# Kernel tuning notes

Measured on AMD Instinct MI355X. Metric: run time of the kernel, lower is better.

## Reference

```python
import jax, jax.numpy as jnp
import numpy as np


def gin_conv(h, src, dst, w1, w2):
    # GINConv, eps=0: mlp(x_i + sum_{j->i} x_j); PyG flow source->target
    agg = jax.ops.segment_sum(h[src], dst, num_segments=h.shape[0])
    z = h + agg
    # create_mlp: Linear(no bias) -> ReLU -> Linear(no bias)
    return jnp.maximum(z @ w1, 0.0) @ w2


def setup_inputs() -> dict:
    N, E, FEAT, D, L, G, OUT = 50000, 800000, 128, 128, 3, 256, 256
    key = jax.random.key(0)
    ks = jax.random.split(key, 8)
    x = jax.random.normal(ks[0], (N, FEAT), jnp.float32)
    edge_index = jax.random.randint(ks[1], (2, E), 0, N, jnp.int32)
    batch_index = jnp.sort(jax.random.randint(ks[2], (N,), 0, G, jnp.int32))
    init = lambda k, shp, fan: jax.random.normal(k, shp, jnp.float32) * np.float32(1.0 / np.sqrt(fan))
    w1_0 = init(ks[3], (FEAT, D), FEAT)
    w2_0 = init(ks[4], (D, D), D)
    gin_w1 = init(ks[5], (L - 1, D, D), D)
    gin_w2 = init(ks[6], (L - 1, D, D), D)
    out_w = init(ks[7], (3 * D, OUT), 3 * D)
    out_b = jnp.zeros((OUT,), jnp.float32)
    return dict(x=x, edge_index=edge_index, batch_index=batch_index,
                w1_0=w1_0, w2_0=w2_0, gin_w1=gin_w1, gin_w2=gin_w2,
                out_w=out_w, out_b=out_b, num_graphs=G)


def reference(x, edge_index, batch_index, w1_0, w2_0, gin_w1, gin_w2, out_w, out_b, num_graphs):
    src, dst = edge_index[0], edge_index[1]
    # dropout is identity in eval mode; batchnorm is unused in the original forward
    h = jnp.maximum(gin_conv(x, src, dst, w1_0, w2_0), 0.0)
    for i in range(gin_w1.shape[0]):  # small fixed layer count
        h = jnp.maximum(gin_conv(h, src, dst, gin_w1[i], gin_w2[i]), 0.0)
    # multi-pool readout: [gmp | gap | gadp]
    gsum = jax.ops.segment_sum(h, batch_index, num_segments=num_graphs)
    cnt = jax.ops.segment_sum(jnp.ones((h.shape[0], 1), h.dtype), batch_index, num_segments=num_graphs)
    gmean = gsum / jnp.maximum(cnt, 1.0)
    gmax = jax.ops.segment_max(h, batch_index, num_segments=num_graphs)
    pooled = jnp.concatenate([gmax, gmean, gsum], axis=1)  # [G, 3*D]
    return pooled @ out_w + out_b
```

## Files before the change

kernel.cpp:

```cpp
#include <hip/hip_runtime.h>

#define DD 128
#define BIN_CH 2048

typedef __attribute__((ext_vector_type(8))) short short8;
typedef __attribute__((ext_vector_type(4))) float f32x4;

__device__ __forceinline__ unsigned short f2bf(float x) {
  unsigned int b = __float_as_uint(x);
  b += 0x7fffu + ((b >> 16) & 1u);
  return (unsigned short)(b >> 16);
}

__device__ __forceinline__ unsigned int cvt_pk_bf16(float lo, float hi) {
  unsigned int d;
  asm("v_cvt_pk_bf16_f32 %0, %1, %2" : "=v"(d) : "v"(lo), "v"(hi));
  return d;
}

__global__ __launch_bounds__(256) void bhist_kernel(const int* __restrict__ dst,
                                                    int* __restrict__ cnt, int E, int NB) {
  __shared__ int lh[256];
  const int t = threadIdx.x;
  lh[t] = 0;
  __syncthreads();
  const int e4 = E >> 2;
  const int4* d4 = (const int4*)dst;
  for (int i = blockIdx.x * 256 + t; i < e4; i += gridDim.x * 256) {
    int4 v = d4[i];
    atomicAdd(&lh[v.x >> 8], 1);
    atomicAdd(&lh[v.y >> 8], 1);
    atomicAdd(&lh[v.z >> 8], 1);
    atomicAdd(&lh[v.w >> 8], 1);
  }
  if (blockIdx.x == 0) {
    for (int i = (e4 << 2) + t; i < E; i += 256) atomicAdd(&lh[dst[i] >> 8], 1);
  }
  __syncthreads();
  if (t < NB && lh[t]) atomicAdd(&cnt[t], lh[t]);
}

__global__ __launch_bounds__(256) void bscan_kernel(const int* __restrict__ cnt,
                                                    int* __restrict__ bucket_base,
                                                    int* __restrict__ cursor,
                                                    int* __restrict__ offs, int NB, int N) {
  __shared__ int s[256];
  const int t = threadIdx.x;
  int v = (t < NB) ? cnt[t] : 0;
  s[t] = v;
  __syncthreads();
#pragma unroll
  for (int o = 1; o < 256; o <<= 1) {
    int u = (t >= o) ? s[t - o] : 0;
    __syncthreads();
    s[t] += u;
    __syncthreads();
  }
  if (t < NB) {
    bucket_base[t] = s[t] - v;
    cursor[t] = s[t] - v;
  }
  if (t == 255) {
    bucket_base[NB] = s[255];
    offs[N] = s[255];
  }
}

__global__ __launch_bounds__(256) void bin_kernel(const int* __restrict__ src,
                                                  const int* __restrict__ dst,
                                                  int* __restrict__ cursor,
                                                  unsigned int* __restrict__ binned,
                                                  int E, int NB) {
  __shared__ int lcount[256], lbase[256], lcur[256], lgbase[256], sscan[256];
  __shared__ unsigned int stage[BIN_CH];
  const int t = threadIdx.x;
  const int cb = blockIdx.x * BIN_CH;
  lcount[t] = 0;
  __syncthreads();

  int sv[BIN_CH / 256], dv[BIN_CH / 256];
#pragma unroll
  for (int i = 0; i < BIN_CH / 256; ++i) {
    const int idx = cb + i * 256 + t;
    if (idx < E) {
      sv[i] = src[idx];
      dv[i] = dst[idx];
      atomicAdd(&lcount[dv[i] >> 8], 1);
    } else {
      sv[i] = -1;
    }
  }
  __syncthreads();
  sscan[t] = lcount[t];
  __syncthreads();
#pragma unroll
  for (int o = 1; o < 256; o <<= 1) {
    int u = (t >= o) ? sscan[t - o] : 0;
    __syncthreads();
    sscan[t] += u;
    __syncthreads();
  }
  lbase[t] = sscan[t] - lcount[t];
  lcur[t] = lbase[t];
  __syncthreads();
#pragma unroll
  for (int i = 0; i < BIN_CH / 256; ++i) {
    if (sv[i] >= 0) {
      const int b = dv[i] >> 8;
      const int pos = atomicAdd(&lcur[b], 1);
      stage[pos] = (unsigned)sv[i] | ((unsigned)(dv[i] & 255) << 16) | ((unsigned)b << 24);
    }
  }
  __syncthreads();
  if (t < NB && lcount[t]) lgbase[t] = atomicAdd(&cursor[t], lcount[t]);
  __syncthreads();
  const int total = (cb + BIN_CH <= E) ? BIN_CH : (E - cb);
  for (int idx = t; idx < total; idx += 256) {
    const unsigned int rec = stage[idx];
    const int b = rec >> 24;
    binned[lgbase[b] + (idx - lbase[b])] = rec;
  }
}

__global__ __launch_bounds__(256) void build_kernel(const unsigned int* __restrict__ binned,
                                                    const int* __restrict__ bucket_base,
                                                    int* __restrict__ csr,
                                                    int* __restrict__ offs, int N) {
  __shared__ int ncount[256], ncur[256], sscan[256];
  const int b = blockIdx.x;
  const int t = threadIdx.x;
  const int nstart = b << 8;
  const int rb = bucket_base[b], re = bucket_base[b + 1];
  ncount[t] = 0;
  __syncthreads();
  for (int idx = rb + t; idx < re; idx += 256)
    atomicAdd(&ncount[(binned[idx] >> 16) & 255], 1);
  __syncthreads();
  sscan[t] = ncount[t];
  __syncthreads();
#pragma unroll
  for (int o = 1; o < 256; o <<= 1) {
    int u = (t >= o) ? sscan[t - o] : 0;
    __syncthreads();
    sscan[t] += u;
    __syncthreads();
  }
  const int excl = sscan[t] - ncount[t];
  ncur[t] = excl;
  if (nstart + t < N) offs[nstart + t] = rb + excl;
  __syncthreads();
  for (int idx = rb + t; idx < re; idx += 256) {
    const unsigned int rec = binned[idx];
    const int p = atomicAdd(&ncur[(rec >> 16) & 255], 1);
    csr[rb + p] = (int)(rec & 0xffffu);
  }
}

__global__ __launch_bounds__(256) void cvt_x_kernel(const float* __restrict__ X,
                                                    unsigned int* __restrict__ Xb, int n4) {
  int i = blockIdx.x * 256 + threadIdx.x;
  if (i >= n4) return;
  float4 v = ((const float4*)X)[i];
  uint2 o;
  o.x = cvt_pk_bf16(v.x, v.y);
  o.y = cvt_pk_bf16(v.z, v.w);
  ((uint2*)Xb)[i] = o;
}

__global__ __launch_bounds__(256) void pack_w_kernel(const float* __restrict__ W,
                                                     unsigned short* __restrict__ P,
                                                     int nmats) {
  int q = blockIdx.x * 256 + threadIdx.x;
  if (q >= nmats * 16384) return;
  int mat = q >> 14;
  int r = q & 16383;
  int e = r & 7, l = (r >> 3) & 63, ks = (r >> 9) & 3, ct = r >> 11;
  int k = ks * 32 + (l >> 4) * 8 + e;
  int n = ct * 16 + (l & 15);
  P[q] = f2bf(W[(size_t)mat * 16384 + k * DD + n]);
}

__global__ __launch_bounds__(256) void pack_wo_kernel(const float* __restrict__ W,
                                                      unsigned short* __restrict__ P) {
  int q = blockIdx.x * 256 + threadIdx.x;
  if (q >= 384 * 256) return;
  int e = q & 7, l = (q >> 3) & 63;
  int rest = q >> 9;
  int ks = rest % 12, ct = rest / 12;
  int k = ks * 32 + (l >> 4) * 8 + e;
  int n = ct * 16 + (l & 15);
  P[q] = f2bf(W[(size_t)k * 256 + n]);
}

__device__ __forceinline__ void bfacc8(float* a, uint4 v) {
  a[0] += __uint_as_float(v.x << 16);
  a[1] += __uint_as_float(v.x & 0xffff0000u);
  a[2] += __uint_as_float(v.y << 16);
  a[3] += __uint_as_float(v.y & 0xffff0000u);
  a[4] += __uint_as_float(v.z << 16);
  a[5] += __uint_as_float(v.z & 0xffff0000u);
  a[6] += __uint_as_float(v.w << 16);
  a[7] += __uint_as_float(v.w & 0xffff0000u);
}

__global__ __launch_bounds__(256) void gin_layer_kernel(
    const uint4* __restrict__ H4, const int* __restrict__ offs,
    const int* __restrict__ csr_src,
    const unsigned short* __restrict__ W1p,
    const unsigned short* __restrict__ W2p,
    unsigned short* __restrict__ Hout, int N) {
  __shared__ unsigned short zl[32 * DD];
  __shared__ unsigned short h1[32 * DD];
  const int t = threadIdx.x;
  const int w = t >> 6;
  const int l = t & 63;
  const int qw = l >> 4;
  const int ql = l & 15;
  const int row0 = blockIdx.x * 32;

#pragma unroll
  for (int i = 0; i < 8; ++i) {
    const int mrow = w * 8 + i;
    const int node = row0 + mrow;
    float acc[8] = {0.f, 0.f, 0.f, 0.f, 0.f, 0.f, 0.f, 0.f};
    if (node < N) {
      if (qw == 0) bfacc8(acc, H4[(size_t)node * 16 + ql]);
      const int e1 = offs[node + 1];
      int e = offs[node] + qw;
      for (; e + 4 < e1; e += 8) {
        uint4 a = H4[(size_t)csr_src[e] * 16 + ql];
        uint4 b = H4[(size_t)csr_src[e + 4] * 16 + ql];
        bfacc8(acc, a);
        bfacc8(acc, b);
      }
      if (e < e1) bfacc8(acc, H4[(size_t)csr_src[e] * 16 + ql]);
    }
#pragma unroll
    for (int j = 0; j < 8; ++j) {
      acc[j] += __shfl_xor(acc[j], 16, 64);
      acc[j] += __shfl_xor(acc[j], 32, 64);
    }
    if (qw == 0) {
      uint4 o;
      o.x = cvt_pk_bf16(acc[0], acc[1]);
      o.y = cvt_pk_bf16(acc[2], acc[3]);
      o.z = cvt_pk_bf16(acc[4], acc[5]);
      o.w = cvt_pk_bf16(acc[6], acc[7]);
      *(uint4*)&zl[mrow * DD + ((ql ^ (mrow & 7)) << 3)] = o;
    }
  }
  __syncthreads();

  const int m_a = l & 15;
  const int g = l >> 4;

  f32x4 acc1[2][2];
#pragma unroll
  for (int t2 = 0; t2 < 2; ++t2)
#pragma unroll
    for (int j = 0; j < 2; ++j) acc1[t2][j] = (f32x4){0.f, 0.f, 0.f, 0.f};

#pragma unroll
  for (int ks = 0; ks < 4; ++ks) {
    const int c8 = ks * 4 + g;
    short8 a0 = *(const short8*)&zl[m_a * DD + ((c8 ^ (m_a & 7)) << 3)];
    short8 a1 = *(const short8*)&zl[(16 + m_a) * DD + ((c8 ^ (m_a & 7)) << 3)];
#pragma unroll
    for (int j = 0; j < 2; ++j) {
      const int ct = w * 2 + j;
      short8 b = *(const short8*)&W1p[(size_t)((ct * 4 + ks) * 64 + l) * 8];
      acc1[0][j] = __builtin_amdgcn_mfma_f32_16x16x32_bf16(a0, b, acc1[0][j], 0, 0, 0);
      acc1[1][j] = __builtin_amdgcn_mfma_f32_16x16x32_bf16(a1, b, acc1[1][j], 0, 0, 0);
    }
  }
#pragma unroll
  for (int t2 = 0; t2 < 2; ++t2)
#pragma unroll
    for (int j = 0; j < 2; ++j) {
      const int c = (w * 2 + j) * 16 + m_a;
#pragma unroll
      for (int r = 0; r < 4; r += 2) {
        unsigned int p = cvt_pk_bf16(fmaxf(acc1[t2][j][r], 0.f),
                                     fmaxf(acc1[t2][j][r + 1], 0.f));
        const int m0 = t2 * 16 + g * 4 + r;
        const int m1 = m0 + 1;
        h1[m0 * DD + (((c >> 3) ^ (m0 & 7)) << 3) + (c & 7)] = (unsigned short)p;
        h1[m1 * DD + (((c >> 3) ^ (m1 & 7)) << 3) + (c & 7)] = (unsigned short)(p >> 16);
      }
    }
  __syncthreads();

  f32x4 acc2[2][2];
#pragma unroll
  for (int t2 = 0; t2 < 2; ++t2)
#pragma unroll
    for (int j = 0; j < 2; ++j) acc2[t2][j] = (f32x4){0.f, 0.f, 0.f, 0.f};

#pragma unroll
  for (int ks = 0; ks < 4; ++ks) {
    const int c8 = ks * 4 + g;
    short8 a0 = *(const short8*)&h1[m_a * DD + ((c8 ^ (m_a & 7)) << 3)];
    short8 a1 = *(const short8*)&h1[(16 + m_a) * DD + ((c8 ^ (m_a & 7)) << 3)];
#pragma unroll
    for (int j = 0; j < 2; ++j) {
      const int ct = w * 2 + j;
      short8 b = *(const short8*)&W2p[(size_t)((ct * 4 + ks) * 64 + l) * 8];
      acc2[0][j] = __builtin_amdgcn_mfma_f32_16x16x32_bf16(a0, b, acc2[0][j], 0, 0, 0);
      acc2[1][j] = __builtin_amdgcn_mfma_f32_16x16x32_bf16(a1, b, acc2[1][j], 0, 0, 0);
    }
  }
#pragma unroll
  for (int t2 = 0; t2 < 2; ++t2)
#pragma unroll
    for (int j = 0; j < 2; ++j) {
      const int c = (w * 2 + j) * 16 + m_a;
#pragma unroll
      for (int r = 0; r < 4; r += 2) {
        unsigned int p = cvt_pk_bf16(fmaxf(acc2[t2][j][r], 0.f),
                                     fmaxf(acc2[t2][j][r + 1], 0.f));
        const int m0 = t2 * 16 + g * 4 + r;
        const int m1 = m0 + 1;
        zl[m0 * DD + (((c >> 3) ^ (m0 & 7)) << 3) + (c & 7)] = (unsigned short)p;
        zl[m1 * DD + (((c >> 3) ^ (m1 & 7)) << 3) + (c & 7)] = (unsigned short)(p >> 16);
      }
    }
  __syncthreads();

#pragma unroll
  for (int it = 0; it < 2; ++it) {
    const int q = t + it * 256;
    const int m = q >> 4;
    const int c8 = q & 15;
    short8 v = *(const short8*)&zl[m * DD + ((c8 ^ (m & 7)) << 3)];
    *(short8*)(Hout + (size_t)(row0 + m) * DD + c8 * 8) = v;
  }
}

__device__ __forceinline__ int lower_bound_dev(const int* a, int n, int v) {
  int lo = 0, hi = n;
  while (lo < hi) {
    int mid = (lo + hi) >> 1;
    if (a[mid] < v) lo = mid + 1; else hi = mid;
  }
  return lo;
}

__global__ __launch_bounds__(256) void pool_kernel(const unsigned int* __restrict__ H2,
                                                   const int* __restrict__ batch,
                                                   unsigned int* __restrict__ pooled_bf,
                                                   int N) {
  const int g = blockIdx.x;
  __shared__ int sRange[2];
  if (threadIdx.x < 2) sRange[threadIdx.x] = lower_bound_dev(batch, N, g + threadIdx.x);
  __syncthreads();
  const int lo = sRange[0], hi = sRange[1];
  const int cp = threadIdx.x & 63;
  const int sl = threadIdx.x >> 6;
  float sx = 0.f, sy = 0.f, mx = 0.f, my = 0.f;
  for (int r = lo + sl; r < hi; r += 4) {
    unsigned int u = H2[(size_t)r * 64 + cp];
    float a = __uint_as_float(u << 16);
    float b = __uint_as_float(u & 0xffff0000u);
    sx += a; sy += b;
    mx = fmaxf(mx, a); my = fmaxf(my, b);
  }
  __shared__ float sS[3][DD], sM[3][DD];
  if (sl > 0) {
    sS[sl - 1][cp * 2] = sx; sS[sl - 1][cp * 2 + 1] = sy;
    sM[sl - 1][cp * 2] = mx; sM[sl - 1][cp * 2 + 1] = my;
  }
  __syncthreads();
  if (sl == 0) {
#pragma unroll
    for (int j = 0; j < 3; ++j) {
      sx += sS[j][cp * 2]; sy += sS[j][cp * 2 + 1];
      mx = fmaxf(mx, sM[j][cp * 2]); my = fmaxf(my, sM[j][cp * 2 + 1]);
    }
    const float cnt = fmaxf((float)(hi - lo), 1.f);
    const size_t pb = (size_t)g * 192;
    pooled_bf[pb + cp] = cvt_pk_bf16(mx, my);
    pooled_bf[pb + 64 + cp] = cvt_pk_bf16(sx / cnt, sy / cnt);
    pooled_bf[pb + 128 + cp] = cvt_pk_bf16(sx, sy);
  }
}

__global__ __launch_bounds__(256) void final_mfma_kernel(const unsigned short* __restrict__ Pb,
                                                         const unsigned short* __restrict__ Wop,
                                                         const float* __restrict__ bo,
                                                         float* __restrict__ out, int G) {
  const int w = threadIdx.x >> 6;
  const int l = threadIdx.x & 63;
  const int rt = blockIdx.x >> 2;
  const int cg = blockIdx.x & 3;
  const int ct = cg * 4 + w;
  const int row0 = rt * 16;
  const int m_a = l & 15;
  const int g = l >> 4;

  f32x4 acc = (f32x4){0.f, 0.f, 0.f, 0.f};
#pragma unroll
  for (int ks = 0; ks < 12; ++ks) {
    short8 a = *(const short8*)&Pb[((size_t)(row0 + m_a) * 384) + ks * 32 + g * 8];
    short8 b = *(const short8*)&Wop[(size_t)((ct * 12 + ks) * 64 + l) * 8];
    acc = __builtin_amdgcn_mfma_f32_16x16x32_bf16(a, b, acc, 0, 0, 0);
  }

  const int n = ct * 16 + m_a;
  const float bias = bo[n];
#pragma unroll
  for (int r = 0; r < 4; ++r) {
    const int row = row0 + g * 4 + r;
    if (row < G) out[(size_t)row * 256 + n] = acc[r] + bias;
  }
}

extern "C" void kernel_launch(void* const* d_in, const int* in_sizes, int n_in,
                              void* d_out, int out_size, void* d_ws, size_t ws_size,
                              hipStream_t stream) {
  const float* x     = (const float*)d_in[0];
  const int*   ei    = (const int*)d_in[1];
  const int*   batch = (const int*)d_in[2];
  const float* w1_0  = (const float*)d_in[3];
  const float* w2_0  = (const float*)d_in[4];
  const float* gw1   = (const float*)d_in[5];
  const float* gw2   = (const float*)d_in[6];
  const float* out_w = (const float*)d_in[7];
  const float* out_b = (const float*)d_in[8];

  const int N   = in_sizes[0] / DD;
  const int E   = in_sizes[1] / 2;
  const int Lm1 = in_sizes[5] / (DD * DD);
  const int OUT = in_sizes[7] / (3 * DD);
  const int G   = out_size / OUT;

  const int* src = ei;
  const int* dst = ei + E;
  const int NB = (N + 255) >> 8;
  const int nmats = 2 + 2 * Lm1;
  const int Npad = (N + 31) & ~31;
  const int Gpad = (G + 15) & ~15;

  char* p = (char*)d_ws;
  auto take = [&](size_t bytes) -> char* {
    char* r = p;
    p += (bytes + 511) & ~(size_t)511;
    return r;
  };
  int* cnt         = (int*)take((size_t)NB * 4);
  int* bucket_base = (int*)take((size_t)(NB + 1) * 4);
  int* cursor      = (int*)take((size_t)NB * 4);
  unsigned int* binned = (unsigned int*)take((size_t)E * 4);
  int* csr         = (int*)take((size_t)E * 4);
  int* offs        = (int*)take((size_t)(N + 1) * 4);
  unsigned short* packW = (unsigned short*)take((size_t)nmats * 16384 * 2);
  unsigned short* packWo = (unsigned short*)take((size_t)384 * 256 * 2);
  unsigned short* xb    = (unsigned short*)take((size_t)Npad * DD * 2);
  unsigned short* bufA  = (unsigned short*)take((size_t)Npad * DD * 2);
  unsigned short* bufB  = (unsigned short*)take((size_t)Npad * DD * 2);
  unsigned int* pooled_bf = (unsigned int*)take((size_t)Gpad * 192 * 4);

  pack_w_kernel<<<(1 * 16384 + 255) / 256, 256, 0, stream>>>(w1_0, packW, 1);
  pack_w_kernel<<<(1 * 16384 + 255) / 256, 256, 0, stream>>>(w2_0, packW + 16384, 1);
  pack_w_kernel<<<(Lm1 * 16384 + 255) / 256, 256, 0, stream>>>(gw1, packW + 2 * 16384, Lm1);
  pack_w_kernel<<<(Lm1 * 16384 + 255) / 256, 256, 0, stream>>>(gw2, packW + (size_t)(2 + Lm1) * 16384, Lm1);
  pack_wo_kernel<<<(384 * 256 + 255) / 256, 256, 0, stream>>>(out_w, packWo);
  cvt_x_kernel<<<(N * DD / 4 + 255) / 256, 256, 0, stream>>>(x, (unsigned int*)xb, N * DD / 4);

  hipMemsetAsync(cnt, 0, (size_t)NB * 4, stream);
  bhist_kernel<<<196, 256, 0, stream>>>(dst, cnt, E, NB);
  bscan_kernel<<<1, 256, 0, stream>>>(cnt, bucket_base, cursor, offs, NB, N);
  bin_kernel<<<(E + BIN_CH - 1) / BIN_CH, 256, 0, stream>>>(src, dst, cursor, binned, E, NB);
  build_kernel<<<NB, 256, 0, stream>>>(binned, bucket_base, csr, offs, N);

  const int ntiles32 = Npad / 32;
  const unsigned short* hcur = xb;
  unsigned short* bufs[2] = {bufA, bufB};
  for (int l = 0; l <= Lm1; ++l) {
    unsigned short* hout = bufs[l & 1];
    const unsigned short* W1p = packW + (size_t)((l == 0) ? 0 : (2 + (l - 1))) * 16384;
    const unsigned short* W2p = packW + (size_t)((l == 0) ? 1 : (2 + Lm1 + (l - 1))) * 16384;
    gin_layer_kernel<<<ntiles32, 256, 0, stream>>>(
        (const uint4*)hcur, offs, csr, W1p, W2p, hout, N);
    hcur = hout;
  }

  pool_kernel<<<G, 256, 0, stream>>>((const unsigned int*)hcur, batch, pooled_bf, N);
  final_mfma_kernel<<<(Gpad / 16) * 4, 256, 0, stream>>>(
      (const unsigned short*)pooled_bf, packWo, out_b, (float*)d_out, G);
}
```

Before: 191.0 us.

## Fuse prep kernels, store CSR as 16-bit, and give each row its own 16-lane group

```diff
diff --git a/kernel.cpp b/kernel.cpp
--- a/kernel.cpp
+++ b/kernel.cpp
@@ -124,7 +124,7 @@
 
 __global__ __launch_bounds__(256) void build_kernel(const unsigned int* __restrict__ binned,
                                                     const int* __restrict__ bucket_base,
-                                                    int* __restrict__ csr,
+                                                    unsigned short* __restrict__ csr16,
                                                     int* __restrict__ offs, int N) {
   __shared__ int ncount[256], ncur[256], sscan[256];
   const int b = blockIdx.x;
@@ -152,44 +152,54 @@
   for (int idx = rb + t; idx < re; idx += 256) {
     const unsigned int rec = binned[idx];
     const int p = atomicAdd(&ncur[(rec >> 16) & 255], 1);
-    csr[rb + p] = (int)(rec & 0xffffu);
-  }
-}
-
-__global__ __launch_bounds__(256) void cvt_x_kernel(const float* __restrict__ X,
-                                                    unsigned int* __restrict__ Xb, int n4) {
-  int i = blockIdx.x * 256 + threadIdx.x;
-  if (i >= n4) return;
-  float4 v = ((const float4*)X)[i];
-  uint2 o;
-  o.x = cvt_pk_bf16(v.x, v.y);
-  o.y = cvt_pk_bf16(v.z, v.w);
-  ((uint2*)Xb)[i] = o;
-}
-
-__global__ __launch_bounds__(256) void pack_w_kernel(const float* __restrict__ W,
-                                                     unsigned short* __restrict__ P,
-                                                     int nmats) {
+    csr16[rb + p] = (unsigned short)(rec & 0xffffu);
+  }
+}
+
+__global__ __launch_bounds__(256) void prep_kernel(
+    const float* __restrict__ x, const float* __restrict__ w1_0,
+    const float* __restrict__ w2_0, const float* __restrict__ gw1,
+    const float* __restrict__ gw2, const float* __restrict__ out_w,
+    unsigned int* __restrict__ xb, unsigned short* __restrict__ packW,
+    unsigned short* __restrict__ packWo, int* __restrict__ cnt,
+    int n4, int nmats, int Lm1, int NB) {
   int q = blockIdx.x * 256 + threadIdx.x;
-  if (q >= nmats * 16384) return;
-  int mat = q >> 14;
-  int r = q & 16383;
-  int e = r & 7, l = (r >> 3) & 63, ks = (r >> 9) & 3, ct = r >> 11;
-  int k = ks * 32 + (l >> 4) * 8 + e;
-  int n = ct * 16 + (l & 15);
-  P[q] = f2bf(W[(size_t)mat * 16384 + k * DD + n]);
-}
-
-__global__ __launch_bounds__(256) void pack_wo_kernel(const float* __restrict__ W,
-                                                      unsigned short* __restrict__ P) {
-  int q = blockIdx.x * 256 + threadIdx.x;
-  if (q >= 384 * 256) return;
-  int e = q & 7, l = (q >> 3) & 63;
-  int rest = q >> 9;
-  int ks = rest % 12, ct = rest / 12;
-  int k = ks * 32 + (l >> 4) * 8 + e;
-  int n = ct * 16 + (l & 15);
-  P[q] = f2bf(W[(size_t)k * 256 + n]);
+  if (q < n4) {
+    float4 v = ((const float4*)x)[q];
+    uint2 o;
+    o.x = cvt_pk_bf16(v.x, v.y);
+    o.y = cvt_pk_bf16(v.z, v.w);
+    ((uint2*)xb)[q] = o;
+    return;
+  }
+  q -= n4;
+  const int npack = nmats * 16384;
+  if (q < npack) {
+    const int mat = q >> 14;
+    const float* W;
+    if (mat == 0) W = w1_0;
+    else if (mat == 1) W = w2_0;
+    else if (mat < 2 + Lm1) W = gw1 + (size_t)(mat - 2) * 16384;
+    else W = gw2 + (size_t)(mat - 2 - Lm1) * 16384;
+    const int r = q & 16383;
+    const int e = r & 7, l = (r >> 3) & 63, ks = (r >> 9) & 3, ct = r >> 11;
+    const int k = ks * 32 + (l >> 4) * 8 + e;
+    const int n = ct * 16 + (l & 15);
+    packW[q] = f2bf(W[(size_t)k * DD + n]);
+    return;
+  }
+  q -= npack;
+  if (q < 384 * 256) {
+    const int e = q & 7, l = (q >> 3) & 63;
+    const int rest = q >> 9;
+    const int ks = rest % 12, ct = rest / 12;
+    const int k = ks * 32 + (l >> 4) * 8 + e;
+    const int n = ct * 16 + (l & 15);
+    packWo[q] = f2bf(out_w[(size_t)k * 256 + n]);
+    return;
+  }
+  q -= 384 * 256;
+  if (q < NB) cnt[q] = 0;
 }
 
 __device__ __forceinline__ void bfacc8(float* a, uint4 v) {
@@ -205,52 +215,49 @@
 
 __global__ __launch_bounds__(256) void gin_layer_kernel(
     const uint4* __restrict__ H4, const int* __restrict__ offs,
-    const int* __restrict__ csr_src,
+    const unsigned short* __restrict__ csr16,
     const unsigned short* __restrict__ W1p,
     const unsigned short* __restrict__ W2p,
     unsigned short* __restrict__ Hout, int N) {
   __shared__ unsigned short zl[32 * DD];
   __shared__ unsigned short h1[32 * DD];
   const int t = threadIdx.x;
-  const int w = t >> 6;
-  const int l = t & 63;
-  const int qw = l >> 4;
-  const int ql = l & 15;
+  const int quarter = t >> 4;
+  const int ql = t & 15;
   const int row0 = blockIdx.x * 32;
 
 #pragma unroll
-  for (int i = 0; i < 8; ++i) {
-    const int mrow = w * 8 + i;
+  for (int i = 0; i < 2; ++i) {
+    const int mrow = quarter + i * 16;
     const int node = row0 + mrow;
     float acc[8] = {0.f, 0.f, 0.f, 0.f, 0.f, 0.f, 0.f, 0.f};
     if (node < N) {
-      if (qw == 0) bfacc8(acc, H4[(size_t)node * 16 + ql]);
+      bfacc8(acc, H4[(size_t)node * 16 + ql]);
       const int e1 = offs[node + 1];
-      int e = offs[node] + qw;
-      for (; e + 4 < e1; e += 8) {
-        uint4 a = H4[(size_t)csr_src[e] * 16 + ql];
-        uint4 b = H4[(size_t)csr_src[e + 4] * 16 + ql];
+      int e = offs[node];
+      for (; e + 3 < e1; e += 4) {
+        uint4 a = H4[(size_t)csr16[e] * 16 + ql];
+        uint4 b = H4[(size_t)csr16[e + 1] * 16 + ql];
+        uint4 c = H4[(size_t)csr16[e + 2] * 16 + ql];
+        uint4 d = H4[(size_t)csr16[e + 3] * 16 + ql];
         bfacc8(acc, a);
         bfacc8(acc, b);
+        bfacc8(acc, c);
+        bfacc8(acc, d);
       }
-      if (e < e1) bfacc8(acc, H4[(size_t)csr_src[e] * 16 + ql]);
-    }
-#pragma unroll
-    for (int j = 0; j < 8; ++j) {
-      acc[j] += __shfl_xor(acc[j], 16, 64);
-      acc[j] += __shfl_xor(acc[j], 32, 64);
-    }
-    if (qw == 0) {
-      uint4 o;
-      o.x = cvt_pk_bf16(acc[0], acc[1]);
-      o.y = cvt_pk_bf16(acc[2], acc[3]);
-      o.z = cvt_pk_bf16(acc[4], acc[5]);
-      o.w = cvt_pk_bf16(acc[6], acc[7]);
-      *(uint4*)&zl[mrow * DD + ((ql ^ (mrow & 7)) << 3)] = o;
-    }
-  }
-  __syncthreads();
-
+      for (; e < e1; ++e) bfacc8(acc, H4[(size_t)csr16[e] * 16 + ql]);
+    }
+    uint4 o;
+    o.x = cvt_pk_bf16(acc[0], acc[1]);
+    o.y = cvt_pk_bf16(acc[2], acc[3]);
+    o.z = cvt_pk_bf16(acc[4], acc[5]);
+    o.w = cvt_pk_bf16(acc[6], acc[7]);
+    *(uint4*)&zl[mrow * DD + ((ql ^ (mrow & 7)) << 3)] = o;
+  }
+  __syncthreads();
+
+  const int w = t >> 6;
+  const int l = t & 63;
   const int m_a = l & 15;
   const int g = l >> 4;
 
@@ -450,7 +457,7 @@
   int* bucket_base = (int*)take((size_t)(NB + 1) * 4);
   int* cursor      = (int*)take((size_t)NB * 4);
   unsigned int* binned = (unsigned int*)take((size_t)E * 4);
-  int* csr         = (int*)take((size_t)E * 4);
+  unsigned short* csr16 = (unsigned short*)take((size_t)E * 2);
   int* offs        = (int*)take((size_t)(N + 1) * 4);
   unsigned short* packW = (unsigned short*)take((size_t)nmats * 16384 * 2);
   unsigned short* packWo = (unsigned short*)take((size_t)384 * 256 * 2);
@@ -459,18 +466,16 @@
   unsigned short* bufB  = (unsigned short*)take((size_t)Npad * DD * 2);
   unsigned int* pooled_bf = (unsigned int*)take((size_t)Gpad * 192 * 4);
 
-  pack_w_kernel<<<(1 * 16384 + 255) / 256, 256, 0, stream>>>(w1_0, packW, 1);
-  pack_w_kernel<<<(1 * 16384 + 255) / 256, 256, 0, stream>>>(w2_0, packW + 16384, 1);
-  pack_w_kernel<<<(Lm1 * 16384 + 255) / 256, 256, 0, stream>>>(gw1, packW + 2 * 16384, Lm1);
-  pack_w_kernel<<<(Lm1 * 16384 + 255) / 256, 256, 0, stream>>>(gw2, packW + (size_t)(2 + Lm1) * 16384, Lm1);
-  pack_wo_kernel<<<(384 * 256 + 255) / 256, 256, 0, stream>>>(out_w, packWo);
-  cvt_x_kernel<<<(N * DD / 4 + 255) / 256, 256, 0, stream>>>(x, (unsigned int*)xb, N * DD / 4);
-
-  hipMemsetAsync(cnt, 0, (size_t)NB * 4, stream);
+  const int n4 = N * DD / 4;
+  const int prep_total = n4 + nmats * 16384 + 384 * 256 + NB;
+  prep_kernel<<<(prep_total + 255) / 256, 256, 0, stream>>>(
+      x, w1_0, w2_0, gw1, gw2, out_w, (unsigned int*)xb, packW, packWo, cnt,
+      n4, nmats, Lm1, NB);
+
   bhist_kernel<<<196, 256, 0, stream>>>(dst, cnt, E, NB);
   bscan_kernel<<<1, 256, 0, stream>>>(cnt, bucket_base, cursor, offs, NB, N);
   bin_kernel<<<(E + BIN_CH - 1) / BIN_CH, 256, 0, stream>>>(src, dst, cursor, binned, E, NB);
-  build_kernel<<<NB, 256, 0, stream>>>(binned, bucket_base, csr, offs, N);
+  build_kernel<<<NB, 256, 0, stream>>>(binned, bucket_base, csr16, offs, N);
 
   const int ntiles32 = Npad / 32;
   const unsigned short* hcur = xb;
@@ -480,7 +485,7 @@
     const unsigned short* W1p = packW + (size_t)((l == 0) ? 0 : (2 + (l - 1))) * 16384;
     const unsigned short* W2p = packW + (size_t)((l == 0) ? 1 : (2 + Lm1 + (l - 1))) * 16384;
     gin_layer_kernel<<<ntiles32, 256, 0, stream>>>(
-        (const uint4*)hcur, offs, csr, W1p, W2p, hout, N);
+        (const uint4*)hcur, offs, csr16, W1p, W2p, hout, N);
     hcur = hout;
   }
 
```

Result: faster. 166.2 us (-13.0%).
